# Performance work log

Hardware: AMD Instinct MI355X
Metric: run time of the kernel (lower is better)

Reference implementation:

```python
import jax, jax.numpy as jnp
import numpy as np

N_HEAD = 16
D_MODEL = 1024
HEAD_DIM = D_MODEL // N_HEAD


def setup_inputs() -> dict:
    key = jax.random.key(0)
    ks = jax.random.split(key, 12)
    B, S, D = 2, 2048, D_MODEL
    scale = 1.0 / np.sqrt(D)
    inp = {
        "q": jax.random.normal(ks[0], (B, S, D), jnp.float32),
        "k": jax.random.normal(ks[1], (B, S, D), jnp.float32),
        "v": jax.random.normal(ks[2], (B, S, D), jnp.float32),
        "mask": jax.random.randint(ks[3], (B, 1, S, S), 0, 2, jnp.int32),
        "wq": jax.random.normal(ks[4], (D, D), jnp.float32) * scale,
        "bq": jnp.zeros((D,), jnp.float32),
        "wk": jax.random.normal(ks[5], (D, D), jnp.float32) * scale,
        "bk": jnp.zeros((D,), jnp.float32),
        "wv": jax.random.normal(ks[6], (D, D), jnp.float32) * scale,
        "bv": jnp.zeros((D,), jnp.float32),
        "wo": jax.random.normal(ks[7], (D, D), jnp.float32) * scale,
        "bo": jnp.zeros((D,), jnp.float32),
    }
    return inp


def _split_heads(x):
    B, S, D = x.shape
    return x.reshape(B, S, N_HEAD, HEAD_DIM).transpose(0, 2, 1, 3)  # [B,H,S,Hd]


def reference(q, k, v, mask, wq, bq, wk, bk, wv, bv, wo, bo):
    _q = _split_heads(q @ wq + bq)
    _k = _split_heads(k @ wk + bk)
    _v = _split_heads(v @ wv + bv)
    inv = 1.0 / (jnp.sqrt(jnp.float32(HEAD_DIM)) + 1e-8)
    score = jnp.einsum("bhqd,bhkd->bhqk", _q, _k) * inv
    score = score + mask.astype(score.dtype) * (-1e9)
    attn = jax.nn.softmax(score, axis=-1)
    ctx = jnp.einsum("bhqk,bhkd->bhqd", attn, _v)
    B, H, S, Hd = ctx.shape
    ctx = ctx.transpose(0, 2, 1, 3).reshape(B, S, H * Hd)
    return ctx @ wo + bo  # dropout is identity (eval / drop_rate=0)
```

## Files before the change

### kernel.cpp

```cpp
#include <hip/hip_runtime.h>

typedef unsigned short u16;
typedef __bf16 bf16x8_t __attribute__((ext_vector_type(8)));
typedef float  f32x4_t  __attribute__((ext_vector_type(4)));
typedef u16    us8_t    __attribute__((ext_vector_type(8)));
typedef u16    us4_t    __attribute__((ext_vector_type(4)));

__device__ __forceinline__ u16 f2bf(float f) {
    __bf16 h = (__bf16)f;
    return __builtin_bit_cast(u16, h);
}
__device__ __forceinline__ bf16x8_t ld_bf8(const u16* p) {
    us8_t u = *(const us8_t*)p;
    return __builtin_bit_cast(bf16x8_t, u);
}
__device__ __forceinline__ f32x4_t mfma16(bf16x8_t a, bf16x8_t b, f32x4_t c) {
    return __builtin_amdgcn_mfma_f32_16x16x32_bf16(a, b, c, 0, 0, 0);
}
__device__ __forceinline__ float exp2_fast(float x) {
#if __has_builtin(__builtin_amdgcn_exp2f)
    return __builtin_amdgcn_exp2f(x);
#else
    return exp2f(x);
#endif
}

__device__ __forceinline__ void dma16(const u16* g, u16* l) {
#if __has_builtin(__builtin_amdgcn_global_load_lds)
    __builtin_amdgcn_global_load_lds((const __attribute__((address_space(1))) unsigned int*)(g),
                                     (__attribute__((address_space(3))) unsigned int*)(l), 16, 0, 0);
#else
    *(us8_t*)l = *(const us8_t*)g;
#endif
}

__global__ __launch_bounds__(256) void prep_kernel(
    const int* __restrict__ mask,
    const float* __restrict__ w0, const float* __restrict__ w1,
    const float* __restrict__ w2, const float* __restrict__ w3,
    u16* __restrict__ Wt, unsigned* __restrict__ mp)
{
    __shared__ u16 t[64][65];
    const int bid = blockIdx.x, tid = threadIdx.x;
    if (bid < 1024) {
        const int z = bid >> 8, rem = bid & 255;
        const float* src = (z == 0) ? w0 : (z == 1) ? w1 : (z == 2) ? w2 : w3;
        u16* dst = Wt + (size_t)z * 1048576;
        const int bk = (rem & 15) * 64, bn = (rem >> 4) * 64;
        const int r = tid >> 2, c4 = tid & 3;
        for (int i = 0; i < 4; i++) {
            float4 vv = *(const float4*)(src + (size_t)(bk + r) * 1024 + bn + c4 * 16 + i * 4);
            t[r][c4 * 16 + i * 4 + 0] = f2bf(vv.x);
            t[r][c4 * 16 + i * 4 + 1] = f2bf(vv.y);
            t[r][c4 * 16 + i * 4 + 2] = f2bf(vv.z);
            t[r][c4 * 16 + i * 4 + 3] = f2bf(vv.w);
        }
        __syncthreads();
        for (int i = 0; i < 2; i++) {
            us8_t w;
            for (int j = 0; j < 8; j++) w[j] = t[c4 * 16 + i * 8 + j][r];
            *(us8_t*)(dst + (size_t)(bn + r) * 1024 + bk + c4 * 16 + i * 8) = w;
        }
    } else {
        const int w = (bid - 1024) * 256 + tid;
        const int* src = mask + (size_t)w * 32;
        unsigned bits = 0u;
        for (int i = 0; i < 32; i += 4) {
            int4 vv = *(const int4*)(src + i);
            bits |= (unsigned)(vv.x != 0) << (i + 0);
            bits |= (unsigned)(vv.y != 0) << (i + 1);
            bits |= (unsigned)(vv.z != 0) << (i + 2);
            bits |= (unsigned)(vv.w != 0) << (i + 3);
        }
        mp[w] = bits;
    }
}

__global__ __launch_bounds__(256) void qkv_gemm_kernel(
    const float* __restrict__ q, const float* __restrict__ k, const float* __restrict__ v,
    const u16* __restrict__ Wt,
    const float* __restrict__ bq, const float* __restrict__ bk, const float* __restrict__ bv,
    u16* __restrict__ Qh, u16* __restrict__ Kh, u16* __restrict__ Vtt)
{
    __shared__ __align__(16) u16 As[2][4096];
    __shared__ __align__(16) u16 Bs[2][4096];
    const int z = blockIdx.z;
    const float* A = (z == 0) ? q : (z == 1) ? k : v;
    const u16* W = Wt + (size_t)z * 1048576;
    const float* bias = (z == 0) ? bq : (z == 1) ? bk : bv;

    const int m0 = blockIdx.x * 128, n0 = blockIdx.y * 128;
    const int tid = threadIdx.x, lane = tid & 63, wave = tid >> 6;
    const int l15 = lane & 15, quad = lane >> 4;
    const int wm = (wave & 1) * 64, wn = (wave >> 1) * 64;
    const int srow = lane >> 2, scol = (lane & 3) * 8;

    const f32x4_t z4 = {0.f, 0.f, 0.f, 0.f};
    f32x4_t acc[4][4];
    for (int i = 0; i < 4; i++) for (int j = 0; j < 4; j++) acc[i][j] = z4;

    float4 ar[2][2];

    auto loadA = [&](int t) {
        const int k0 = t * 32;
        #pragma unroll
        for (int i = 0; i < 2; i++) {
            const float* src = A + (size_t)(m0 + wave * 32 + i * 16 + srow) * 1024 + k0 + scol;
            ar[i][0] = *(const float4*)src;
            ar[i][1] = *(const float4*)(src + 4);
        }
    };
    auto writeA = [&](int bs) {
        #pragma unroll
        for (int i = 0; i < 2; i++) {
            us8_t w8;
            w8[0] = f2bf(ar[i][0].x); w8[1] = f2bf(ar[i][0].y);
            w8[2] = f2bf(ar[i][0].z); w8[3] = f2bf(ar[i][0].w);
            w8[4] = f2bf(ar[i][1].x); w8[5] = f2bf(ar[i][1].y);
            w8[6] = f2bf(ar[i][1].z); w8[7] = f2bf(ar[i][1].w);
            *(us8_t*)&As[bs][wave * 1024 + i * 512 + lane * 8] = w8;
        }
    };
    auto stageW = [&](int t, int bs) {
        const int k0 = t * 32;
        #pragma unroll
        for (int i = 0; i < 2; i++)
            dma16(W + (size_t)(n0 + wave * 32 + i * 16 + srow) * 1024 + k0 + scol,
                  &Bs[bs][wave * 1024 + i * 512 + lane * 8]);
    };

    stageW(0, 0);
    loadA(0);
    writeA(0);

    for (int t = 0; t < 32; ++t) {
        const int bs = t & 1;
        __syncthreads();
        if (t < 31) {
            stageW(t + 1, bs ^ 1);
            loadA(t + 1);
        }

        bf16x8_t af[4], bfr[4];
        #pragma unroll
        for (int i = 0; i < 4; i++) af[i] = ld_bf8(&As[bs][(wm + i * 16 + l15) * 32 + quad * 8]);
        #pragma unroll
        for (int j = 0; j < 4; j++) bfr[j] = ld_bf8(&Bs[bs][(wn + j * 16 + l15) * 32 + quad * 8]);
        #pragma unroll
        for (int i = 0; i < 4; i++)
            #pragma unroll
            for (int j = 0; j < 4; j++)
                acc[i][j] = mfma16(af[i], bfr[j], acc[i][j]);

        if (t < 31) writeA(bs ^ 1);
    }

    #pragma unroll
    for (int i = 0; i < 4; i++) {
        const int m = m0 + wm + i * 16 + quad * 4;
        #pragma unroll
        for (int j = 0; j < 4; j++) {
            const int gn = n0 + wn + j * 16 + l15;
            const float bb = bias[gn];
            const int h = gn >> 6, dh = gn & 63;
            if (z < 2) {
                u16* Y = z ? Kh : Qh;
                const int jc = dh >> 3, e = dh & 7;
                #pragma unroll
                for (int r = 0; r < 4; r++) {
                    const int mm = m + r;
                    const int b = mm >> 11, s = mm & 2047;
                    Y[((size_t)(b * 16 + h) * 2048 + s) * 64 + ((jc ^ (s & 7)) * 8) + e] =
                        f2bf(acc[i][j][r] + bb);
                }
            } else {
                const int b = m >> 11, sh = m & 2047, kt2 = sh >> 7, sl = sh & 127;
                const int poslow = ((sl >> 4) & 1) * 4;
                const int chunk = (sl >> 5) * 4 + ((sl >> 2) & 3);
                us4_t w4;
                #pragma unroll
                for (int r = 0; r < 4; r++) w4[r] = f2bf(acc[i][j][r] + bb);
                size_t off = (((size_t)(b * 16 + h) * 16 + kt2) * 8192)
                           + (size_t)dh * 128 + ((chunk ^ (dh & 7)) * 8) + poslow;
                *(us4_t*)&Vtt[off] = w4;
            }
        }
    }
}

__global__ __launch_bounds__(256) void out_gemm_kernel(
    const u16* __restrict__ X, const u16* __restrict__ Wt,
    const float* __restrict__ bias, float* __restrict__ Y)
{
    __shared__ __align__(16) u16 As[2][2048];
    __shared__ __align__(16) u16 Bs[2][4096];
    const int m0 = blockIdx.x * 64, n0 = blockIdx.y * 128;
    const int tid = threadIdx.x, lane = tid & 63, wave = tid >> 6;
    const int l15 = lane & 15, quad = lane >> 4;
    const int wm = (wave & 1) * 32, wn = (wave >> 1) * 64;
    const int srow = lane >> 2, scol = (lane & 3) * 8;

    const f32x4_t z4 = {0.f, 0.f, 0.f, 0.f};
    f32x4_t acc[2][4];
    for (int i = 0; i < 2; i++) for (int j = 0; j < 4; j++) acc[i][j] = z4;

    auto stage = [&](int t, int bs) {
        const int k0 = t * 32;
        dma16(X + (size_t)(m0 + wave * 16 + srow) * 1024 + k0 + scol,
              &As[bs][wave * 512 + lane * 8]);
        #pragma unroll
        for (int i = 0; i < 2; i++)
            dma16(Wt + (size_t)(n0 + wave * 32 + i * 16 + srow) * 1024 + k0 + scol,
                  &Bs[bs][wave * 1024 + i * 512 + lane * 8]);
    };

    stage(0, 0);

    for (int t = 0; t < 32; ++t) {
        const int bs = t & 1;
        __syncthreads();
        if (t < 31) stage(t + 1, bs ^ 1);

        bf16x8_t af[2], bfr[4];
        #pragma unroll
        for (int i = 0; i < 2; i++) af[i] = ld_bf8(&As[bs][(wm + i * 16 + l15) * 32 + quad * 8]);
        #pragma unroll
        for (int j = 0; j < 4; j++) bfr[j] = ld_bf8(&Bs[bs][(wn + j * 16 + l15) * 32 + quad * 8]);
        #pragma unroll
        for (int i = 0; i < 2; i++)
            #pragma unroll
            for (int j = 0; j < 4; j++)
                acc[i][j] = mfma16(af[i], bfr[j], acc[i][j]);
    }

    #pragma unroll
    for (int i = 0; i < 2; i++) {
        const int m = m0 + wm + i * 16 + quad * 4;
        #pragma unroll
        for (int j = 0; j < 4; j++) {
            const int gn = n0 + wn + j * 16 + l15;
            const float bb = bias[gn];
            #pragma unroll
            for (int r = 0; r < 4; r++)
                Y[(size_t)(m + r) * 1024 + gn] = acc[i][j][r] + bb;
        }
    }
}

__global__ __launch_bounds__(256, 4) void attn_kernel(
    const u16* __restrict__ Qh, const u16* __restrict__ Kh,
    const u16* __restrict__ Vtt, const unsigned* __restrict__ mp,
    u16* __restrict__ C)
{
    __shared__ __align__(16) u16 Ks[2][4096];
    __shared__ __align__(16) u16 Vs[2][4096];
    __shared__ __align__(16) float4 lut[16];
    const int h = blockIdx.x, qb = blockIdx.y, b = blockIdx.z;
    const int tid = threadIdx.x, lane = tid & 63, wave = tid >> 6;
    const int l15 = lane & 15, quad = lane >> 4;
    const int q0 = qb * 64 + wave * 16;
    const int grow = b * 2048 + q0;
    const size_t headoff = (size_t)(b * 16 + h) * 131072;
    const u16* Qg = Qh + headoff;
    const u16* Kg = Kh + headoff;
    const u16* Vg = Vtt + headoff;

    if (tid < 16) {
        float4 bv4;
        bv4.x = (tid & 1) ? -1e5f : -17.312340491f;
        bv4.y = (tid & 2) ? -1e5f : -17.312340491f;
        bv4.z = (tid & 4) ? -1e5f : -17.312340491f;
        bv4.w = (tid & 8) ? -1e5f : -17.312340491f;
        lut[tid] = bv4;
    }

    bf16x8_t aq[2];
    #pragma unroll
    for (int ks = 0; ks < 2; ks++)
        aq[ks] = ld_bf8(Qg + (size_t)(q0 + l15) * 64 + (((ks * 4 + quad) ^ (l15 & 7)) * 8));

    us8_t ones_u;
    #pragma unroll
    for (int i = 0; i < 8; i++) ones_u[i] = 0x3F80;
    const bf16x8_t ones = __builtin_bit_cast(bf16x8_t, ones_u);

    const f32x4_t z4 = {0.f, 0.f, 0.f, 0.f};
    f32x4_t o[4];
    #pragma unroll
    for (int i = 0; i < 4; i++) o[i] = z4;
    f32x4_t osum = z4;

    const int swA = (quad ^ (l15 & 7)) * 8;
    const int swB = ((4 + quad) ^ (l15 & 7)) * 8;

    const unsigned* mrow = mp + (size_t)(b * 2048 + q0 + l15) * 64;

    auto stage = [&](int kt, int bs) {
        const u16* kg = Kg + kt * 4096 + wave * 1024;
        const u16* vg = Vg + (kt >> 1) * 8192 + (kt & 1) * 64;
        u16* kl = &Ks[bs][wave * 1024];
        u16* vl = &Vs[bs][wave * 1024];
        #pragma unroll
        for (int i = 0; i < 2; i++) {
            dma16(kg + i * 512 + lane * 8, kl + i * 512 + lane * 8);
            dma16(vg + (size_t)(wave * 16 + i * 8 + (lane >> 3)) * 128 + (lane & 7) * 8,
                  vl + i * 512 + lane * 8);
        }
    };

    stage(0, 0);

    for (int kt = 0; kt < 32; ++kt) {
        const int bs = kt & 1;
        __syncthreads();
        if (kt < 31) stage(kt + 1, bs ^ 1);

        const int2 mv = *(const int2*)(mrow + kt * 2);

        f32x4_t sc[4];
        __builtin_amdgcn_s_setprio(1);
        #pragma unroll
        for (int st = 0; st < 4; st++) {
            const u16* kp = &Ks[bs][(st * 16 + l15) * 64];
            bf16x8_t k0 = ld_bf8(kp + swA);
            bf16x8_t k1 = ld_bf8(kp + swB);
            sc[st] = mfma16(k1, aq[1], mfma16(k0, aq[0], z4));
        }
        __builtin_amdgcn_s_setprio(0);

        us8_t ap[2];
        #pragma unroll
        for (int st = 0; st < 4; st++) {
            const unsigned w = (st < 2) ? (unsigned)mv.x : (unsigned)mv.y;
            const int nib = (w >> (((st & 1) << 4) + quad * 4)) & 15;
            const float4 b4 = lut[nib];
            ap[st >> 1][((st & 1) << 2) + 0] = f2bf(exp2_fast(fmaf(sc[st][0], 0.18033688011f, b4.x)));
            ap[st >> 1][((st & 1) << 2) + 1] = f2bf(exp2_fast(fmaf(sc[st][1], 0.18033688011f, b4.y)));
            ap[st >> 1][((st & 1) << 2) + 2] = f2bf(exp2_fast(fmaf(sc[st][2], 0.18033688011f, b4.z)));
            ap[st >> 1][((st & 1) << 2) + 3] = f2bf(exp2_fast(fmaf(sc[st][3], 0.18033688011f, b4.w)));
        }

        __builtin_amdgcn_s_setprio(1);
        #pragma unroll
        for (int c = 0; c < 2; c++) {
            bf16x8_t a = __builtin_bit_cast(bf16x8_t, ap[c]);
            osum = mfma16(a, ones, osum);
            #pragma unroll
            for (int nt = 0; nt < 4; nt++) {
                bf16x8_t bv = ld_bf8(&Vs[bs][(nt * 16 + l15) * 64
                                             + (((c * 4 + quad) ^ (l15 & 7)) * 8)]);
                o[nt] = mfma16(a, bv, o[nt]);
            }
        }
        __builtin_amdgcn_s_setprio(0);
    }

    #pragma unroll
    for (int r = 0; r < 4; r++) {
        const float invl = 1.0f / osum[r];
        const int row = grow + quad * 4 + r;
        #pragma unroll
        for (int nt = 0; nt < 4; nt++)
            C[(size_t)row * 1024 + h * 64 + nt * 16 + l15] = f2bf(o[nt][r] * invl);
    }
}

extern "C" void kernel_launch(void* const* d_in, const int* in_sizes, int n_in,
                              void* d_out, int out_size, void* d_ws, size_t ws_size,
                              hipStream_t stream) {
    const float* q    = (const float*)d_in[0];
    const float* k    = (const float*)d_in[1];
    const float* v    = (const float*)d_in[2];
    const int*   mask = (const int*)d_in[3];
    const float* wq   = (const float*)d_in[4];
    const float* bq   = (const float*)d_in[5];
    const float* wk   = (const float*)d_in[6];
    const float* bk   = (const float*)d_in[7];
    const float* wv   = (const float*)d_in[8];
    const float* bv   = (const float*)d_in[9];
    const float* wo   = (const float*)d_in[10];
    const float* bo   = (const float*)d_in[11];
    float* out = (float*)d_out;

    char* ws = (char*)d_ws;
    const size_t MB = 1ull << 20;
    u16* Wt      = (u16*)(ws);
    u16* Qhh     = (u16*)(ws + 8 * MB);
    u16* Khh     = (u16*)(ws + 16 * MB);
    u16* Vtt     = (u16*)(ws + 24 * MB);
    u16* CT      = (u16*)(ws + 32 * MB);
    unsigned* mp = (unsigned*)(ws + 40 * MB);

    prep_kernel<<<dim3(2048), 256, 0, stream>>>(
        mask, wq, wk, wv, wo, Wt, mp);

    qkv_gemm_kernel<<<dim3(32, 8, 3), 256, 0, stream>>>(
        q, k, v, Wt, bq, bk, bv, Qhh, Khh, Vtt);

    attn_kernel<<<dim3(16, 32, 2), 256, 0, stream>>>(Qhh, Khh, Vtt, mp, CT);

    out_gemm_kernel<<<dim3(64, 8), 256, 0, stream>>>(CT, Wt + 3ull * 1048576, bo, out);
}
```

Before: 270.2 us.

## Load QKV GEMM operands directly from global into registers, dropping LDS staging

The QKV projection GEMM no longer stages A and W tiles through shared memory with barriers. Each lane loads its MFMA fragments straight from global memory into registers and prefetches the next k-slice one iteration ahead. This removes LDS writes, LDS reads and __syncthreads, but each operand row is now fetched separately by both waves that need it, doubling global and cache traffic. The per-lane loads are also only 32 bytes per row, which coalesces poorly.

New measurement: 332.2 us. 1.23x slower.

```diff
diff --git a/kernel.cpp b/kernel.cpp
--- a/kernel.cpp
+++ b/kernel.cpp
@@ -82,8 +82,6 @@
     const float* __restrict__ bq, const float* __restrict__ bk, const float* __restrict__ bv,
     u16* __restrict__ Qh, u16* __restrict__ Kh, u16* __restrict__ Vtt)
 {
-    __shared__ __align__(16) u16 As[2][4096];
-    __shared__ __align__(16) u16 Bs[2][4096];
     const int z = blockIdx.z;
     const float* A = (z == 0) ? q : (z == 1) ? k : v;
     const u16* W = Wt + (size_t)z * 1048576;
@@ -93,66 +91,56 @@
     const int tid = threadIdx.x, lane = tid & 63, wave = tid >> 6;
     const int l15 = lane & 15, quad = lane >> 4;
     const int wm = (wave & 1) * 64, wn = (wave >> 1) * 64;
-    const int srow = lane >> 2, scol = (lane & 3) * 8;
+
+    const float* arow[4];
+    const u16*   wrow[4];
+    #pragma unroll
+    for (int i = 0; i < 4; i++)
+        arow[i] = A + (size_t)(m0 + wm + i * 16 + l15) * 1024 + quad * 8;
+    #pragma unroll
+    for (int j = 0; j < 4; j++)
+        wrow[j] = W + (size_t)(n0 + wn + j * 16 + l15) * 1024 + quad * 8;
 
     const f32x4_t z4 = {0.f, 0.f, 0.f, 0.f};
     f32x4_t acc[4][4];
     for (int i = 0; i < 4; i++) for (int j = 0; j < 4; j++) acc[i][j] = z4;
 
-    float4 ar[2][2];
-
-    auto loadA = [&](int t) {
+    float4 a0r[4], a1r[4];
+    us8_t  wr[4];
+    auto LD = [&](int t) {
         const int k0 = t * 32;
         #pragma unroll
-        for (int i = 0; i < 2; i++) {
-            const float* src = A + (size_t)(m0 + wave * 32 + i * 16 + srow) * 1024 + k0 + scol;
-            ar[i][0] = *(const float4*)src;
-            ar[i][1] = *(const float4*)(src + 4);
-        }
+        for (int i = 0; i < 4; i++) {
+            a0r[i] = *(const float4*)(arow[i] + k0);
+            a1r[i] = *(const float4*)(arow[i] + k0 + 4);
+        }
+        #pragma unroll
+        for (int j = 0; j < 4; j++) wr[j] = *(const us8_t*)(wrow[j] + k0);
     };
-    auto writeA = [&](int bs) {
-        #pragma unroll
-        for (int i = 0; i < 2; i++) {
+
+    LD(0);
+
+    for (int t = 0; t < 32; ++t) {
+        bf16x8_t af[4], bfr[4];
+        #pragma unroll
+        for (int i = 0; i < 4; i++) {
             us8_t w8;
-            w8[0] = f2bf(ar[i][0].x); w8[1] = f2bf(ar[i][0].y);
-            w8[2] = f2bf(ar[i][0].z); w8[3] = f2bf(ar[i][0].w);
-            w8[4] = f2bf(ar[i][1].x); w8[5] = f2bf(ar[i][1].y);
-            w8[6] = f2bf(ar[i][1].z); w8[7] = f2bf(ar[i][1].w);
-            *(us8_t*)&As[bs][wave * 1024 + i * 512 + lane * 8] = w8;
-        }
-    };
-    auto stageW = [&](int t, int bs) {
-        const int k0 = t * 32;
-        #pragma unroll
-        for (int i = 0; i < 2; i++)
-            dma16(W + (size_t)(n0 + wave * 32 + i * 16 + srow) * 1024 + k0 + scol,
-                  &Bs[bs][wave * 1024 + i * 512 + lane * 8]);
-    };
-
-    stageW(0, 0);
-    loadA(0);
-    writeA(0);
-
-    for (int t = 0; t < 32; ++t) {
-        const int bs = t & 1;
-        __syncthreads();
-        if (t < 31) {
-            stageW(t + 1, bs ^ 1);
-            loadA(t + 1);
-        }
-
-        bf16x8_t af[4], bfr[4];
-        #pragma unroll
-        for (int i = 0; i < 4; i++) af[i] = ld_bf8(&As[bs][(wm + i * 16 + l15) * 32 + quad * 8]);
-        #pragma unroll
-        for (int j = 0; j < 4; j++) bfr[j] = ld_bf8(&Bs[bs][(wn + j * 16 + l15) * 32 + quad * 8]);
+            w8[0] = f2bf(a0r[i].x); w8[1] = f2bf(a0r[i].y);
+            w8[2] = f2bf(a0r[i].z); w8[3] = f2bf(a0r[i].w);
+            w8[4] = f2bf(a1r[i].x); w8[5] = f2bf(a1r[i].y);
+            w8[6] = f2bf(a1r[i].z); w8[7] = f2bf(a1r[i].w);
+            af[i] = __builtin_bit_cast(bf16x8_t, w8);
+        }
+        #pragma unroll
+        for (int j = 0; j < 4; j++) bfr[j] = __builtin_bit_cast(bf16x8_t, wr[j]);
+
+        if (t < 31) LD(t + 1);
+
         #pragma unroll
         for (int i = 0; i < 4; i++)
             #pragma unroll
             for (int j = 0; j < 4; j++)
                 acc[i][j] = mfma16(af[i], bfr[j], acc[i][j]);
-
-        if (t < 31) writeA(bs ^ 1);
     }
 
     #pragma unroll
```
